# Optimization experiments

Hardware: AMD Instinct MI355X
Metric: run time of the kernel (lower is better)

Reference implementation:

```python
import jax, jax.numpy as jnp
import numpy as np

B, N = 16384, 4096
NBLOCKS = 4
BLK = N // NBLOCKS  # 1024


def setup_inputs() -> dict:
    key = jax.random.key(0)
    kx, k1, k2, kb = jax.random.split(key, 4)
    # match torch kaiming-style uniform bounds approximately; exact init values
    # don't affect correctness testing, scale kept modest for stability
    bound_w = float(np.sqrt(3.0) * (np.sqrt(2.0 / (1 + 5)) / np.sqrt(BLK)))
    bound_b = 1.0 / float(np.sqrt(N))
    x = jax.random.normal(kx, (B, N), dtype=jnp.float32)
    w1 = jax.random.uniform(k1, (NBLOCKS, BLK, BLK), jnp.float32, -bound_w, bound_w)
    w2 = jax.random.uniform(k2, (NBLOCKS, BLK, BLK), jnp.float32, -bound_w, bound_w)
    bias = jax.random.uniform(kb, (N,), jnp.float32, -bound_b, bound_b)
    return {"x": x, "w1": w1, "w2": w2, "bias": bias}


def monarch_matmul(x, w1, w2):
    # x: (B, n); w1: (k, q, p) with k*p = n; w2: (l, s, r) with l*r = k*q
    Bd, n = x.shape
    k, q, p = w1.shape
    l, s, r = w2.shape
    # out1[b,k,q] = sum_p x[b,k,p] * w1[k,q,p]
    out1 = jnp.einsum('bkp,kqp->bkq', x.reshape(Bd, k, p), w1)
    # permute (k*q) flat -> (r, l), then transpose to (l, r)
    t = out1.reshape(Bd, r, l).transpose(0, 2, 1)  # (B, l, r)
    # out2[b,l,s] = sum_r t[b,l,r] * w2[l,s,r]
    out2 = jnp.einsum('blr,lsr->bls', t, w2)
    # permute to (B, s, l) then flatten -> (B, s*l)
    return out2.transpose(0, 2, 1).reshape(Bd, s * l)


def reference(x, w1, w2, bias):
    return monarch_matmul(x, w1, w2) + bias
```

## Files before the change

kernel.cpp:

```cpp
#include <hip/hip_runtime.h>
#include <hip/hip_bf16.h>
#include <stdint.h>

typedef __bf16 bf16_t;
typedef bf16_t bf16x8 __attribute__((ext_vector_type(8)));
typedef bf16_t bf16x4 __attribute__((ext_vector_type(4)));
typedef float  f32x4  __attribute__((ext_vector_type(4)));

#define B_DIM 16384

#define BAR()    __builtin_amdgcn_s_barrier()
#define MEMF()   asm volatile("" ::: "memory")
#define VMCNT6() asm volatile("s_waitcnt vmcnt(6)" ::: "memory")
#define VMCNT0() asm volatile("s_waitcnt vmcnt(0)" ::: "memory")

__device__ __forceinline__ void async_copy16(void* lptr, const void* gptr) {
  __builtin_amdgcn_global_load_lds(
      (const __attribute__((address_space(1))) unsigned int*)gptr,
      (__attribute__((address_space(3))) unsigned int*)lptr, 16, 0, 0);
}

__global__ void cast_all_kernel(const float* __restrict__ x, const float* __restrict__ w1,
                                const float* __restrict__ w2, bf16_t* __restrict__ xb,
                                bf16_t* __restrict__ w1b, bf16_t* __restrict__ w2b) {
  size_t c = (size_t)blockIdx.x * 256 + threadIdx.x;
  const float* s; bf16_t* d; size_t off;
  if (c < 8388608)      { s = x;  d = xb;  off = c; }
  else if (c < 8912896) { s = w1; d = w1b; off = c - 8388608; }
  else                  { s = w2; d = w2b; off = c - 8912896; }
  size_t i = off * 8;
  f32x4 a = *(const f32x4*)(s + i);
  f32x4 b = *(const f32x4*)(s + i + 4);
  bf16x8 o;
  o[0]=(bf16_t)a[0]; o[1]=(bf16_t)a[1]; o[2]=(bf16_t)a[2]; o[3]=(bf16_t)a[3];
  o[4]=(bf16_t)b[0]; o[5]=(bf16_t)b[1]; o[6]=(bf16_t)b[2]; o[7]=(bf16_t)b[3];
  *(bf16x8*)(d + i) = o;
}

template<int EPI>
__global__ __launch_bounds__(512, 2)
void monarch_gemm8(const bf16_t* __restrict__ Ab, const bf16_t* __restrict__ Wb,
                   bf16_t* __restrict__ Outb)
{
  __shared__ __align__(16) char smem[131072];
  const int tid  = threadIdx.x;
  const int lane = tid & 63;
  const int wid  = tid >> 6;
  const int wm   = wid >> 2;
  const int wn   = wid & 3;

  const int pb = blockIdx.x;
  const int lb = (pb & 7) * 128 + (pb >> 3);
  const int zi = lb >> 8;
  const int mt = (lb & 255) >> 2;
  const int nt = lb & 3;

  const size_t brow0 = (size_t)mt * 256;
  const int    ncol0 = nt * 256;

  const bf16_t* Asrc = Ab + brow0 * 4096 + (size_t)zi * 1024;
  const bf16_t* Bsrc = Wb + ((size_t)zi << 20) + (size_t)ncol0 * 1024;

  const int sRow = lane >> 3;
  const int sC   = (lane & 7) ^ sRow;

#define STAGE(BUF, T, H) do {                                                   \
    const bf16_t* _s = (H) < 2 ? Asrc + ((size_t)((H) * 128) * 4096) + (T) * 64 \
                               : Bsrc + ((size_t)(((H)-2) * 128) * 1024) + (T) * 64; \
    const size_t _st = (H) < 2 ? 4096 : 1024;                                   \
    async_copy16(smem + (BUF)*65536 + ((H)>>1)*32768 + ((H)&1)*16384 + wid*1024,\
                 _s + (size_t)(wid * 8 + sRow) * _st + sC * 8);                 \
    async_copy16(smem + (BUF)*65536 + ((H)>>1)*32768 + ((H)&1)*16384 + 8192 + wid*1024, \
                 _s + (size_t)(64 + wid * 8 + sRow) * _st + sC * 8);            \
  } while (0)

  const int cs0 = ((0 + (lane >> 4)) ^ (lane & 7)) * 16;
  const int cs1 = ((4 + (lane >> 4)) ^ (lane & 7)) * 16;
  const int aBase = (wm * 128 + (lane & 15)) * 128;
  const int bBase = 32768 + (wn * 64 + (lane & 15)) * 128;

#define RDA(buf, m, kk) (*(const bf16x8*)(smem + (buf)*65536 + aBase + (m)*2048 + ((kk)?cs1:cs0)))
#define RDB(buf, n, kk) (*(const bf16x8*)(smem + (buf)*65536 + bBase + (n)*2048 + ((kk)?cs1:cs0)))

  f32x4 acc[8][4] = {};
  bf16x8 aM0[4][2], aM1[4][2], bN0[2][2], bN1[2][2];

#define MFMA_QUAD(AR, Aarr, NB, Barr)                                              \
  __builtin_amdgcn_s_setprio(1);                                                   \
  _Pragma("unroll") for (int m = 0; m < 4; ++m)                                    \
  _Pragma("unroll") for (int n = 0; n < 2; ++n)                                    \
  _Pragma("unroll") for (int kk = 0; kk < 2; ++kk)                                 \
    acc[(AR)+m][(NB)+n] = __builtin_amdgcn_mfma_f32_16x16x32_bf16(                 \
        Aarr[m][kk], Barr[n][kk], acc[(AR)+m][(NB)+n], 0, 0, 0);                   \
  __builtin_amdgcn_s_setprio(0);

#define LD_A0(buf) _Pragma("unroll") for (int m = 0; m < 4; ++m) { \
    aM0[m][0] = RDA(buf,m,0); aM0[m][1] = RDA(buf,m,1); }
#define LD_A1(buf) _Pragma("unroll") for (int m = 0; m < 4; ++m) { \
    aM1[m][0] = RDA(buf,m+4,0); aM1[m][1] = RDA(buf,m+4,1); }
#define LD_B0(buf) _Pragma("unroll") for (int n = 0; n < 2; ++n) { \
    bN0[n][0] = RDB(buf,n,0); bN0[n][1] = RDB(buf,n,1); }
#define LD_B1(buf) _Pragma("unroll") for (int n = 0; n < 2; ++n) { \
    bN1[n][0] = RDB(buf,n+2,0); bN1[n][1] = RDB(buf,n+2,1); }

  STAGE(0,0,0); MEMF(); STAGE(0,0,1); MEMF(); STAGE(0,0,2); MEMF(); STAGE(0,0,3); MEMF();
  STAGE(1,1,0); MEMF(); STAGE(1,1,1); MEMF(); STAGE(1,1,2);
  VMCNT6(); BAR();
  LD_B0(0);

  for (int it2 = 0; it2 < 8; ++it2) {
    const int t0 = it2 * 2;
    const bool nl = (it2 < 7);
    LD_A0(0);
    MEMF(); STAGE(1, t0+1, 3);
    BAR();
    MFMA_QUAD(0, aM0, 0, bN0);
    BAR();
    LD_A1(0);
    BAR();
    MFMA_QUAD(4, aM1, 0, bN0);
    BAR();
    LD_B1(0);
    if (nl) { MEMF(); STAGE(0, t0+2, 0); }
    BAR();
    MFMA_QUAD(0, aM0, 2, bN1);
    BAR();
    if (nl) { MEMF(); STAGE(0, t0+2, 1); MEMF(); STAGE(0, t0+2, 2); VMCNT6(); }
    else    { VMCNT0(); }
    BAR();
    LD_B0(1);
    MFMA_QUAD(4, aM1, 2, bN1);
    BAR();
    LD_A0(1);
    if (nl) { MEMF(); STAGE(0, t0+2, 3); }
    BAR();
    MFMA_QUAD(0, aM0, 0, bN0);
    BAR();
    LD_A1(1);
    BAR();
    MFMA_QUAD(4, aM1, 0, bN0);
    BAR();
    LD_B1(1);
    if (nl) { MEMF(); STAGE(1, t0+3, 0); }
    BAR();
    MFMA_QUAD(0, aM0, 2, bN1);
    BAR();
    if (nl) { MEMF(); STAGE(1, t0+3, 1); MEMF(); STAGE(1, t0+3, 2); VMCNT6(); }
    BAR();
    if (nl) { LD_B0(0); }
    MFMA_QUAD(4, aM1, 2, bN1);
    BAR();
  }

  if (EPI == 0) {
    bf16_t* C0 = (bf16_t*)smem;
    #pragma unroll
    for (int half = 0; half < 2; ++half) {
      BAR();
      if (wm == half) {
        const int rg = lane >> 4, cl = lane & 15;
        const int l = cl & 3, rvb = cl >> 2;
        #pragma unroll
        for (int m = 0; m < 8; ++m)
          #pragma unroll
          for (int n = 0; n < 4; ++n) {
            const int rowb = (m * 16 + rg * 4) * 288 + l * 72 + wn * 16 + n * 4 + rvb;
            #pragma unroll
            for (int j = 0; j < 4; ++j)
              C0[rowb + j * 288] = (bf16_t)acc[m][n][j];
          }
      }
      BAR();
      #pragma unroll
      for (int i = 0; i < 8; ++i) {
        const int s = i * 512 + tid;
        const int row = s >> 5, l2 = (s >> 3) & 3, part = s & 7;
        bf16x8 v = *(const bf16x8*)&C0[row * 288 + l2 * 72 + part * 8];
        *(bf16x8*)&Outb[(brow0 + half * 128 + row) * 4096 +
                        l2 * 1024 + zi * 256 + nt * 64 + part * 8] = v;
      }
    }
  } else {
    bf16_t* C = (bf16_t*)smem;
    #pragma unroll
    for (int half = 0; half < 2; ++half) {
      BAR();
      if (wm == half) {
        const int rg = lane >> 4, cl = lane & 15;
        #pragma unroll
        for (int m = 0; m < 8; ++m)
          #pragma unroll
          for (int n = 0; n < 4; ++n) {
            const int rl = m * 16 + rg * 4;
            const int col = wn * 64 + n * 16 + cl;
            #pragma unroll
            for (int j = 0; j < 4; ++j)
              C[(rl + j) * 264 + col] = (bf16_t)acc[m][n][j];
          }
      }
      BAR();
      #pragma unroll
      for (int i = 0; i < 8; ++i) {
        const int s = i * 512 + tid;
        const int row = s >> 5, ch = s & 31;
        bf16x8 v = *(const bf16x8*)&C[row * 264 + ch * 8];
        *(bf16x8*)&Outb[(brow0 + half * 128 + row) * 4096 +
                        (size_t)zi * 1024 + ncol0 + ch * 8] = v;
      }
    }
  }
#undef RDA
#undef RDB
#undef MFMA_QUAD
#undef LD_A0
#undef LD_A1
#undef LD_B0
#undef LD_B1
#undef STAGE
}

__global__ void permute_bias_kernel(const bf16_t* __restrict__ o2,
                                    const float* __restrict__ bias,
                                    float* __restrict__ out) {
  const int t = blockIdx.x * 256 + threadIdx.x;
  const int b = t >> 8;
  const int s0 = (t & 255) * 4;
  const size_t rowb = (size_t)b * 4096;
  bf16x4 vl[4];
  #pragma unroll
  for (int l = 0; l < 4; ++l) vl[l] = *(const bf16x4*)(o2 + rowb + l * 1024 + s0);
  #pragma unroll
  for (int si = 0; si < 4; ++si) {
    f32x4 bb = *(const f32x4*)(bias + (size_t)(s0 + si) * 4);
    f32x4 o;
    o[0] = (float)vl[0][si] + bb[0];
    o[1] = (float)vl[1][si] + bb[1];
    o[2] = (float)vl[2][si] + bb[2];
    o[3] = (float)vl[3][si] + bb[3];
    *(f32x4*)(out + rowb + (size_t)(s0 + si) * 4) = o;
  }
}

extern "C" void kernel_launch(void* const* d_in, const int* in_sizes, int n_in,
                              void* d_out, int out_size, void* d_ws, size_t ws_size,
                              hipStream_t stream) {
  const float* x    = (const float*)d_in[0];
  const float* w1   = (const float*)d_in[1];
  const float* w2   = (const float*)d_in[2];
  const float* bias = (const float*)d_in[3];
  float* out = (float*)d_out;

  char* ws = (char*)d_ws;
  const size_t xbBytes    = (size_t)B_DIM * 4096 * 2;
  const size_t wBytes     = (size_t)8 << 20;
  bf16_t* xb    = (bf16_t*)(ws);
  bf16_t* w1b   = (bf16_t*)(ws + xbBytes);
  bf16_t* w2b   = (bf16_t*)(ws + xbBytes + wBytes);
  bf16_t* inter = (bf16_t*)(ws + xbBytes + 2 * wBytes);
  bf16_t* o2    = xb;

  cast_all_kernel<<<36864, 256, 0, stream>>>(x, w1, w2, xb, w1b, w2b);
  monarch_gemm8<0><<<1024, 512, 0, stream>>>(xb, w1b, inter);
  monarch_gemm8<1><<<1024, 512, 0, stream>>>(inter, w2b, o2);
  permute_bias_kernel<<<16384, 256, 0, stream>>>(o2, bias, out);
}
```

Before: 499.0 us.

## Fuse fp32-to-bf16 cast of x into first monarch GEMM's A loading

Removes the separate cast of the 256MB fp32 input x into a bf16 workspace. The first GEMM now reads fp32 x straight into registers, converts it to bf16, and writes the swizzled tile into LDS, while B tiles still arrive through async global-to-LDS copies. The cast kernel now handles only the weights. This drops one full write and re-read of x, at the cost of register-staged A loads, extra lgkm waits and a more complex pipeline inside the GEMM.

```diff
diff --git a/kernel.cpp b/kernel.cpp
--- a/kernel.cpp
+++ b/kernel.cpp
@@ -9,10 +9,13 @@
 
 #define B_DIM 16384
 
-#define BAR()    __builtin_amdgcn_s_barrier()
-#define MEMF()   asm volatile("" ::: "memory")
-#define VMCNT6() asm volatile("s_waitcnt vmcnt(6)" ::: "memory")
-#define VMCNT0() asm volatile("s_waitcnt vmcnt(0)" ::: "memory")
+#define BAR()     __builtin_amdgcn_s_barrier()
+#define MEMF()    asm volatile("" ::: "memory")
+#define LGKM0()   asm volatile("s_waitcnt lgkmcnt(0)" ::: "memory")
+#define VMCNT6()  asm volatile("s_waitcnt vmcnt(6)" ::: "memory")
+#define VMCNT10() asm volatile("s_waitcnt vmcnt(10)" ::: "memory")
+#define VMCNT12() asm volatile("s_waitcnt vmcnt(12)" ::: "memory")
+#define VMCNT0()  asm volatile("s_waitcnt vmcnt(0)" ::: "memory")
 
 __device__ __forceinline__ void async_copy16(void* lptr, const void* gptr) {
   __builtin_amdgcn_global_load_lds(
@@ -20,26 +23,193 @@
       (__attribute__((address_space(3))) unsigned int*)lptr, 16, 0, 0);
 }
 
-__global__ void cast_all_kernel(const float* __restrict__ x, const float* __restrict__ w1,
-                                const float* __restrict__ w2, bf16_t* __restrict__ xb,
-                                bf16_t* __restrict__ w1b, bf16_t* __restrict__ w2b) {
-  size_t c = (size_t)blockIdx.x * 256 + threadIdx.x;
-  const float* s; bf16_t* d; size_t off;
-  if (c < 8388608)      { s = x;  d = xb;  off = c; }
-  else if (c < 8912896) { s = w1; d = w1b; off = c - 8388608; }
-  else                  { s = w2; d = w2b; off = c - 8912896; }
-  size_t i = off * 8;
-  f32x4 a = *(const f32x4*)(s + i);
-  f32x4 b = *(const f32x4*)(s + i + 4);
+__global__ void cast_w_kernel(const float* __restrict__ w1, const float* __restrict__ w2,
+                              bf16_t* __restrict__ w1b, bf16_t* __restrict__ w2b) {
+  const float* src = blockIdx.y ? w2 : w1;
+  bf16_t* dst = blockIdx.y ? w2b : w1b;
+  size_t i = ((size_t)blockIdx.x * 256 + threadIdx.x) * 8;
+  f32x4 a = *(const f32x4*)(src + i);
+  f32x4 b = *(const f32x4*)(src + i + 4);
   bf16x8 o;
   o[0]=(bf16_t)a[0]; o[1]=(bf16_t)a[1]; o[2]=(bf16_t)a[2]; o[3]=(bf16_t)a[3];
   o[4]=(bf16_t)b[0]; o[5]=(bf16_t)b[1]; o[6]=(bf16_t)b[2]; o[7]=(bf16_t)b[3];
-  *(bf16x8*)(d + i) = o;
-}
-
-template<int EPI>
+  *(bf16x8*)(dst + i) = o;
+}
+
 __global__ __launch_bounds__(512, 2)
-void monarch_gemm8(const bf16_t* __restrict__ Ab, const bf16_t* __restrict__ Wb,
+void monarch_gemm1_f32(const float* __restrict__ Xf, const bf16_t* __restrict__ Wb,
+                       bf16_t* __restrict__ Outb)
+{
+  __shared__ __align__(16) char smem[131072];
+  const int tid  = threadIdx.x;
+  const int lane = tid & 63;
+  const int wid  = tid >> 6;
+  const int wm   = wid >> 2;
+  const int wn   = wid & 3;
+
+  const int pb = blockIdx.x;
+  const int lb = (pb & 7) * 128 + (pb >> 3);
+  const int zi = lb >> 8;
+  const int mt = (lb & 255) >> 2;
+  const int nt = lb & 3;
+
+  const size_t brow0 = (size_t)mt * 256;
+  const int    ncol0 = nt * 256;
+
+  const float*  Axf  = Xf + brow0 * 4096 + (size_t)zi * 1024;
+  const bf16_t* Bsrc = Wb + ((size_t)zi << 20) + (size_t)ncol0 * 1024;
+
+  const int sRow = lane >> 3;
+  const int sC   = (lane & 7) ^ sRow;
+
+#define STAGE(BUF, T, H) do {                                                   \
+    const bf16_t* _s = Bsrc + ((size_t)(((H)-2) * 128) * 1024) + (T) * 64;      \
+    async_copy16(smem + (BUF)*65536 + 32768 + ((H)&1)*16384 + wid*1024,         \
+                 _s + (size_t)(wid * 8 + sRow) * 1024 + sC * 8);                \
+    async_copy16(smem + (BUF)*65536 + 32768 + ((H)&1)*16384 + 8192 + wid*1024,  \
+                 _s + (size_t)(64 + wid * 8 + sRow) * 1024 + sC * 8);           \
+  } while (0)
+
+  const int ar  = (tid >> 3) * 4;
+  const int ac8 = (tid & 7) * 8;
+  f32x4 aw[4][2];
+
+#define ALOAD(T) do { MEMF();                                                   \
+    _Pragma("unroll") for (int q = 0; q < 4; ++q) {                             \
+      const float* _p = Axf + (size_t)(ar + q) * 4096 + (T) * 64 + ac8;         \
+      aw[q][0] = *(const f32x4*)_p; aw[q][1] = *(const f32x4*)(_p + 4); }       \
+    MEMF(); } while (0)
+
+#define ACVT(BUF) do { MEMF();                                                  \
+    _Pragma("unroll") for (int q = 0; q < 4; ++q) {                             \
+      f32x4 _u = aw[q][0], _v = aw[q][1]; bf16x8 _pk;                           \
+      _pk[0]=(bf16_t)_u[0]; _pk[1]=(bf16_t)_u[1]; _pk[2]=(bf16_t)_u[2];         \
+      _pk[3]=(bf16_t)_u[3]; _pk[4]=(bf16_t)_v[0]; _pk[5]=(bf16_t)_v[1];         \
+      _pk[6]=(bf16_t)_v[2]; _pk[7]=(bf16_t)_v[3];                               \
+      const int _r = ar + q;                                                    \
+      *(bf16x8*)(smem + (BUF)*65536 + _r * 128 +                                \
+                 (((tid & 7) ^ (_r & 7)) << 4)) = _pk; }                        \
+    MEMF(); } while (0)
+
+  const int cs0 = ((0 + (lane >> 4)) ^ (lane & 7)) * 16;
+  const int cs1 = ((4 + (lane >> 4)) ^ (lane & 7)) * 16;
+  const int aBase = (wm * 128 + (lane & 15)) * 128;
+  const int bBase = 32768 + (wn * 64 + (lane & 15)) * 128;
+
+#define RDA(buf, m, kk) (*(const bf16x8*)(smem + (buf)*65536 + aBase + (m)*2048 + ((kk)?cs1:cs0)))
+#define RDB(buf, n, kk) (*(const bf16x8*)(smem + (buf)*65536 + bBase + (n)*2048 + ((kk)?cs1:cs0)))
+
+  f32x4 acc[8][4] = {};
+  bf16x8 aM0[4][2], aM1[4][2], bN0[2][2], bN1[2][2];
+
+#define MFMA_QUAD(AR, Aarr, NB, Barr)                                              \
+  __builtin_amdgcn_s_setprio(1);                                                   \
+  _Pragma("unroll") for (int m = 0; m < 4; ++m)                                    \
+  _Pragma("unroll") for (int n = 0; n < 2; ++n)                                    \
+  _Pragma("unroll") for (int kk = 0; kk < 2; ++kk)                                 \
+    acc[(AR)+m][(NB)+n] = __builtin_amdgcn_mfma_f32_16x16x32_bf16(                 \
+        Aarr[m][kk], Barr[n][kk], acc[(AR)+m][(NB)+n], 0, 0, 0);                   \
+  __builtin_amdgcn_s_setprio(0);
+
+#define LD_A0(buf) _Pragma("unroll") for (int m = 0; m < 4; ++m) { \
+    aM0[m][0] = RDA(buf,m,0); aM0[m][1] = RDA(buf,m,1); }
+#define LD_A1(buf) _Pragma("unroll") for (int m = 0; m < 4; ++m) { \
+    aM1[m][0] = RDA(buf,m+4,0); aM1[m][1] = RDA(buf,m+4,1); }
+#define LD_B0(buf) _Pragma("unroll") for (int n = 0; n < 2; ++n) { \
+    bN0[n][0] = RDB(buf,n,0); bN0[n][1] = RDB(buf,n,1); }
+#define LD_B1(buf) _Pragma("unroll") for (int n = 0; n < 2; ++n) { \
+    bN1[n][0] = RDB(buf,n+2,0); bN1[n][1] = RDB(buf,n+2,1); }
+
+  ALOAD(0);
+  ACVT(0);
+  STAGE(0, 0, 2); MEMF(); STAGE(0, 0, 3); MEMF();
+  ALOAD(1);
+  STAGE(1, 1, 2);
+  LGKM0();
+  VMCNT10(); BAR();
+  LD_B0(0);
+
+  for (int it2 = 0; it2 < 8; ++it2) {
+    const int t0 = it2 * 2;
+    const bool nl = (it2 < 7);
+    LD_A0(0);
+    ACVT(1);
+    MEMF(); STAGE(1, t0+1, 3);
+    if (nl) ALOAD(t0+2);
+    LGKM0();
+    BAR();
+    MFMA_QUAD(0, aM0, 0, bN0);
+    BAR();
+    LD_A1(0);
+    BAR(); MFMA_QUAD(4, aM1, 0, bN0); BAR();
+    LD_B1(0);
+    BAR(); MFMA_QUAD(0, aM0, 2, bN1); BAR();
+    if (nl) { MEMF(); STAGE(0, t0+2, 2); VMCNT12(); }
+    else    { VMCNT0(); }
+    BAR();
+    LD_B0(1);
+    MFMA_QUAD(4, aM1, 2, bN1);
+    BAR();
+    LD_A0(1);
+    if (nl) { ACVT(0);
+              MEMF(); STAGE(0, t0+2, 3);
+              ALOAD(t0+3); }
+    LGKM0();
+    BAR();
+    MFMA_QUAD(0, aM0, 0, bN0);
+    BAR();
+    LD_A1(1);
+    BAR(); MFMA_QUAD(4, aM1, 0, bN0); BAR();
+    LD_B1(1);
+    BAR(); MFMA_QUAD(0, aM0, 2, bN1); BAR();
+    if (nl) { MEMF(); STAGE(1, t0+3, 2); VMCNT12(); }
+    BAR();
+    if (nl) { LD_B0(0); }
+    MFMA_QUAD(4, aM1, 2, bN1);
+    BAR();
+  }
+
+  bf16_t* C0 = (bf16_t*)smem;
+  #pragma unroll
+  for (int half = 0; half < 2; ++half) {
+    BAR();
+    if (wm == half) {
+      const int rg = lane >> 4, cl = lane & 15;
+      const int l = cl & 3, rvb = cl >> 2;
+      #pragma unroll
+      for (int m = 0; m < 8; ++m)
+        #pragma unroll
+        for (int n = 0; n < 4; ++n) {
+          const int rowb = (m * 16 + rg * 4) * 288 + l * 72 + wn * 16 + n * 4 + rvb;
+          #pragma unroll
+          for (int j = 0; j < 4; ++j)
+            C0[rowb + j * 288] = (bf16_t)acc[m][n][j];
+        }
+    }
+    BAR();
+    #pragma unroll
+    for (int i = 0; i < 8; ++i) {
+      const int s = i * 512 + tid;
+      const int row = s >> 5, l2 = (s >> 3) & 3, part = s & 7;
+      bf16x8 v = *(const bf16x8*)&C0[row * 288 + l2 * 72 + part * 8];
+      *(bf16x8*)&Outb[(brow0 + half * 128 + row) * 4096 +
+                      l2 * 1024 + zi * 256 + nt * 64 + part * 8] = v;
+    }
+  }
+#undef RDA
+#undef RDB
+#undef MFMA_QUAD
+#undef LD_A0
+#undef LD_A1
+#undef LD_B0
+#undef LD_B1
+#undef STAGE
+#undef ALOAD
+#undef ACVT
+}
+
+__global__ __launch_bounds__(512, 2)
+void monarch_gemm2(const bf16_t* __restrict__ Ab, const bf16_t* __restrict__ Wb,
                    bf16_t* __restrict__ Outb)
 {
   __shared__ __align__(16) char smem[131072];
@@ -117,14 +287,10 @@
     MFMA_QUAD(0, aM0, 0, bN0);
     BAR();
     LD_A1(0);
-    BAR();
-    MFMA_QUAD(4, aM1, 0, bN0);
-    BAR();
+    BAR(); MFMA_QUAD(4, aM1, 0, bN0); BAR();
     LD_B1(0);
     if (nl) { MEMF(); STAGE(0, t0+2, 0); }
-    BAR();
-    MFMA_QUAD(0, aM0, 2, bN1);
-    BAR();
+    BAR(); MFMA_QUAD(0, aM0, 2, bN1); BAR();
     if (nl) { MEMF(); STAGE(0, t0+2, 1); MEMF(); STAGE(0, t0+2, 2); VMCNT6(); }
     else    { VMCNT0(); }
     BAR();
@@ -133,18 +299,12 @@
     BAR();
     LD_A0(1);
     if (nl) { MEMF(); STAGE(0, t0+2, 3); }
-    BAR();
-    MFMA_QUAD(0, aM0, 0, bN0);
-    BAR();
+    BAR(); MFMA_QUAD(0, aM0, 0, bN0); BAR();
     LD_A1(1);
-    BAR();
-    MFMA_QUAD(4, aM1, 0, bN0);
-    BAR();
+    BAR(); MFMA_QUAD(4, aM1, 0, bN0); BAR();
     LD_B1(1);
     if (nl) { MEMF(); STAGE(1, t0+3, 0); }
-    BAR();
-    MFMA_QUAD(0, aM0, 2, bN1);
-    BAR();
+    BAR(); MFMA_QUAD(0, aM0, 2, bN1); BAR();
     if (nl) { MEMF(); STAGE(1, t0+3, 1); MEMF(); STAGE(1, t0+3, 2); VMCNT6(); }
     BAR();
     if (nl) { LD_B0(0); }
@@ -152,61 +312,31 @@
     BAR();
   }
 
-  if (EPI == 0) {
-    bf16_t* C0 = (bf16_t*)smem;
+  bf16_t* C = (bf16_t*)smem;
+  #pragma unroll
+  for (int half = 0; half < 2; ++half) {
+    BAR();
+    if (wm == half) {
+      const int rg = lane >> 4, cl = lane & 15;
+      #pragma unroll
+      for (int m = 0; m < 8; ++m)
+        #pragma unroll
+        for (int n = 0; n < 4; ++n) {
+          const int rl = m * 16 + rg * 4;
+          const int col = wn * 64 + n * 16 + cl;
+          #pragma unroll
+          for (int j = 0; j < 4; ++j)
+            C[(rl + j) * 264 + col] = (bf16_t)acc[m][n][j];
+        }
+    }
+    BAR();
     #pragma unroll
-    for (int half = 0; half < 2; ++half) {
-      BAR();
-      if (wm == half) {
-        const int rg = lane >> 4, cl = lane & 15;
-        const int l = cl & 3, rvb = cl >> 2;
-        #pragma unroll
-        for (int m = 0; m < 8; ++m)
-          #pragma unroll
-          for (int n = 0; n < 4; ++n) {
-            const int rowb = (m * 16 + rg * 4) * 288 + l * 72 + wn * 16 + n * 4 + rvb;
-            #pragma unroll
-            for (int j = 0; j < 4; ++j)
-              C0[rowb + j * 288] = (bf16_t)acc[m][n][j];
-          }
-      }
-      BAR();
-      #pragma unroll
-      for (int i = 0; i < 8; ++i) {
-        const int s = i * 512 + tid;
-        const int row = s >> 5, l2 = (s >> 3) & 3, part = s & 7;
-        bf16x8 v = *(const bf16x8*)&C0[row * 288 + l2 * 72 + part * 8];
-        *(bf16x8*)&Outb[(brow0 + half * 128 + row) * 4096 +
-                        l2 * 1024 + zi * 256 + nt * 64 + part * 8] = v;
-      }
-    }
-  } else {
-    bf16_t* C = (bf16_t*)smem;
-    #pragma unroll
-    for (int half = 0; half < 2; ++half) {
-      BAR();
-      if (wm == half) {
-        const int rg = lane >> 4, cl = lane & 15;
-        #pragma unroll
-        for (int m = 0; m < 8; ++m)
-          #pragma unroll
-          for (int n = 0; n < 4; ++n) {
-            const int rl = m * 16 + rg * 4;
-            const int col = wn * 64 + n * 16 + cl;
-            #pragma unroll
-            for (int j = 0; j < 4; ++j)
-              C[(rl + j) * 264 + col] = (bf16_t)acc[m][n][j];
-          }
-      }
-      BAR();
-      #pragma unroll
-      for (int i = 0; i < 8; ++i) {
-        const int s = i * 512 + tid;
-        const int row = s >> 5, ch = s & 31;
-        bf16x8 v = *(const bf16x8*)&C[row * 264 + ch * 8];
-        *(bf16x8*)&Outb[(brow0 + half * 128 + row) * 4096 +
-                        (size_t)zi * 1024 + ncol0 + ch * 8] = v;
-      }
+    for (int i = 0; i < 8; ++i) {
+      const int s = i * 512 + tid;
+      const int row = s >> 5, ch = s & 31;
+      bf16x8 v = *(const bf16x8*)&C[row * 264 + ch * 8];
+      *(bf16x8*)&Outb[(brow0 + half * 128 + row) * 4096 +
+                      (size_t)zi * 1024 + ncol0 + ch * 8] = v;
     }
   }
 #undef RDA
@@ -251,16 +381,15 @@
   float* out = (float*)d_out;
 
   char* ws = (char*)d_ws;
-  const size_t xbBytes    = (size_t)B_DIM * 4096 * 2;
   const size_t wBytes     = (size_t)8 << 20;
-  bf16_t* xb    = (bf16_t*)(ws);
-  bf16_t* w1b   = (bf16_t*)(ws + xbBytes);
-  bf16_t* w2b   = (bf16_t*)(ws + xbBytes + wBytes);
-  bf16_t* inter = (bf16_t*)(ws + xbBytes + 2 * wBytes);
-  bf16_t* o2    = xb;
-
-  cast_all_kernel<<<36864, 256, 0, stream>>>(x, w1, w2, xb, w1b, w2b);
-  monarch_gemm8<0><<<1024, 512, 0, stream>>>(xb, w1b, inter);
-  monarch_gemm8<1><<<1024, 512, 0, stream>>>(inter, w2b, o2);
+  const size_t interBytes = (size_t)B_DIM * 4096 * 2;
+  bf16_t* w1b   = (bf16_t*)(ws);
+  bf16_t* w2b   = (bf16_t*)(ws + wBytes);
+  bf16_t* inter = (bf16_t*)(ws + 2 * wBytes);
+  bf16_t* o2    = (bf16_t*)(ws + 2 * wBytes + interBytes);
+
+  cast_w_kernel<<<dim3(2048, 2), 256, 0, stream>>>(w1, w2, w1b, w2b);
+  monarch_gemm1_f32<<<1024, 512, 0, stream>>>(x, w1b, inter);
+  monarch_gemm2<<<1024, 512, 0, stream>>>(inter, w2b, o2);
   permute_bias_kernel<<<16384, 256, 0, stream>>>(o2, bias, out);
 }
```

Result: slower. 683.9 us (+37.1%).
